# Kernel optimization log

Measured on AMD Instinct MI355X. Metric: run time of the kernel, lower is better.

The kernel has to match this reference:

```python
import jax, jax.numpy as jnp
import numpy as np

N = 50000       # n_nodes
E = 800000      # n_edges
DIN = 64
DH = 64
DOUT = 64


def setup_inputs() -> dict:
    key = jax.random.key(0)
    k0, k1, k2, k3, k4 = jax.random.split(key, 5)
    x = jax.random.normal(k0, (N, DIN), dtype=jnp.float32)
    edge_index = jax.random.randint(k1, (2, E), 0, N, dtype=jnp.int32)
    # learnable per-edge weight (nn.Parameter); positive init keeps gcn_norm well-defined
    edge_weight = jax.random.uniform(k2, (E,), jnp.float32, 0.1, 1.0)
    W1 = jax.random.normal(k3, (DH, DIN), dtype=jnp.float32) * (1.0 / np.sqrt(DIN))
    b1 = jnp.zeros((DH,), jnp.float32)
    W2 = jax.random.normal(k4, (DOUT, DH), dtype=jnp.float32) * (1.0 / np.sqrt(DH))
    b2 = jnp.zeros((DOUT,), jnp.float32)
    return {"x": x, "edge_weight": edge_weight, "W1": W1, "b1": b1,
            "W2": W2, "b2": b2, "edge_index": edge_index}


def _gcn_norm(edge_index, edge_weight, n):
    # PyG gcn_norm: add self-loops (weight 1), symmetric normalization.
    loop = jnp.arange(n, dtype=edge_index.dtype)
    row = jnp.concatenate([edge_index[0], loop])   # source nodes
    col = jnp.concatenate([edge_index[1], loop])   # target nodes
    w = jnp.concatenate([edge_weight, jnp.ones((n,), edge_weight.dtype)])
    deg = jax.ops.segment_sum(w, col, num_segments=n)
    dinv = jnp.where(deg > 0, jax.lax.rsqrt(jnp.where(deg > 0, deg, 1.0)), 0.0)
    norm = dinv[row] * w * dinv[col]               # [E + N]
    return row, col, norm


def _gcn_layer(x, W, b, row, col, norm, n):
    h = x @ W.T                                     # [N, out]
    # gather source features, scale by norm, scatter-add into targets
    out = jax.ops.segment_sum(h[row] * norm[:, None], col, num_segments=n)
    return out + b


def reference(x, edge_weight, W1, b1, W2, b2, edge_index):
    n = x.shape[0]
    row, col, norm = _gcn_norm(edge_index, edge_weight, n)
    h = _gcn_layer(x, W1, b1, row, col, norm, n)
    h = jax.nn.relu(h)                              # self.pre: ReLU + Dropout (identity in eval)
    return _gcn_layer(h, W2, b2, row, col, norm, n)
```

## Files before the change

### kernel.cpp

```cpp
#include <hip/hip_runtime.h>

#define D 64
#define GN 128
#define SW 68
#define SX 132
#define MAXDEG 64
#define RBITS_C 8
#define RANGE_C 256
#define MAXB_C 5120
#define RANGE_F 64
#define APB 2048

typedef unsigned long long u64;
typedef unsigned int u32;
typedef unsigned short u16;
typedef unsigned char u8;

__device__ __forceinline__ float4 fma4(float4 w, float s, float4 c) {
    c.x = fmaf(w.x, s, c.x); c.y = fmaf(w.y, s, c.y);
    c.z = fmaf(w.z, s, c.z); c.w = fmaf(w.w, s, c.w);
    return c;
}

__device__ __forceinline__ u32 f2bf(float f) {
    u32 u = __float_as_uint(f);
    return (u + 0x7FFFu + ((u >> 16) & 1u)) >> 16;
}
__device__ __forceinline__ u32 pack2(float a, float b) { return f2bf(a) | (f2bf(b) << 16); }
__device__ __forceinline__ float blo(u32 u) { return __uint_as_float(u << 16); }
__device__ __forceinline__ float bhi(u32 u) { return __uint_as_float(u & 0xFFFF0000u); }

__global__ __launch_bounds__(256) void k_g1b(
        const float* __restrict__ in, const float* __restrict__ W,
        u16* __restrict__ h, int N, int GG,
        const int* __restrict__ ei, const float* __restrict__ ew,
        u64* __restrict__ barr, u32* __restrict__ gcount, int E, int NB) {
    __shared__ __align__(16) char smem[51200];
    int t = threadIdx.x;

    if ((int)blockIdx.x < GG) {
        float* sWt = (float*)smem;
        float* sxT = (float*)(smem + 17408);
        int node0 = blockIdx.x * GN;

        for (int i = t; i < D * D / 4; i += 256) {
            int j = i >> 4, k4 = i & 15;
            float4 w = ((const float4*)W)[i];
            sWt[(4 * k4 + 0) * SW + j] = w.x;
            sWt[(4 * k4 + 1) * SW + j] = w.y;
            sWt[(4 * k4 + 2) * SW + j] = w.z;
            sWt[(4 * k4 + 3) * SW + j] = w.w;
        }
        for (int i = t; i < GN * D / 4; i += 256) {
            int nn = i >> 4, k4 = i & 15;
            int n = node0 + nn;
            float4 v = make_float4(0.f, 0.f, 0.f, 0.f);
            if (n < N) v = ((const float4*)(in + (size_t)n * D))[k4];
            sxT[(4 * k4 + 0) * SX + nn] = v.x;
            sxT[(4 * k4 + 1) * SX + nn] = v.y;
            sxT[(4 * k4 + 2) * SX + nn] = v.z;
            sxT[(4 * k4 + 3) * SX + nn] = v.w;
        }
        __syncthreads();

        int jg = (t & 7) * 8;
        int ng = (t >> 3) * 4;
        float4 a0[4], a1[4];
        #pragma unroll
        for (int a = 0; a < 4; ++a) {
            a0[a] = make_float4(0.f, 0.f, 0.f, 0.f);
            a1[a] = make_float4(0.f, 0.f, 0.f, 0.f);
        }

        #pragma unroll 8
        for (int k = 0; k < D; ++k) {
            const float* wr = &sWt[k * SW + jg];
            float4 w0 = *(const float4*)wr;
            float4 w1 = *(const float4*)(wr + 4);
            float4 xv = *(const float4*)&sxT[k * SX + ng];
            a0[0] = fma4(w0, xv.x, a0[0]);  a1[0] = fma4(w1, xv.x, a1[0]);
            a0[1] = fma4(w0, xv.y, a0[1]);  a1[1] = fma4(w1, xv.y, a1[1]);
            a0[2] = fma4(w0, xv.z, a0[2]);  a1[2] = fma4(w1, xv.z, a1[2]);
            a0[3] = fma4(w0, xv.w, a0[3]);  a1[3] = fma4(w1, xv.w, a1[3]);
        }

        #pragma unroll
        for (int a = 0; a < 4; ++a) {
            int n = node0 + ng + a;
            if (n >= N) continue;
            uint4 st;
            st.x = pack2(a0[a].x, a0[a].y);
            st.y = pack2(a0[a].z, a0[a].w);
            st.z = pack2(a1[a].x, a1[a].y);
            st.w = pack2(a1[a].z, a1[a].w);
            *(uint4*)(h + (size_t)n * D + jg) = st;
        }
    } else {
        u64* srec  = (u64*)smem;
        u8*  sbkt  = (u8*)(smem + 16384);
        u32* scnt  = (u32*)(smem + 18432);
        u32* sbase = (u32*)(smem + 19456);

        int e0 = (blockIdx.x - GG) * APB;
        int ne = min(APB, E - e0);

        for (int i = t; i < 256; i += 256) scnt[i] = 0;
        __syncthreads();

        for (int i = t; i < ne; i += 256) {
            int e   = e0 + i;
            int r   = ei[e];
            int c   = ei[(size_t)E + e];
            float w = ew[e];
            int b   = c >> RBITS_C;
            srec[i] = ((u64)__float_as_uint(w) << 32)
                    | (u32)r | ((u32)(c & (RANGE_C - 1)) << 20);
            sbkt[i] = (u8)b;
            atomicAdd(&scnt[b], 1u);
        }
        __syncthreads();

        for (int i = t; i < NB; i += 256) {
            u32 cnt = scnt[i];
            sbase[i] = cnt ? atomicAdd(&gcount[i], cnt) : 0u;
            scnt[i] = 0;
        }
        __syncthreads();

        for (int i = t; i < ne; i += 256) {
            int b   = sbkt[i];
            u32 rk  = atomicAdd(&scnt[b], 1u);
            u32 pos = sbase[b] + rk;
            if (pos < MAXB_C) barr[(size_t)b * MAXB_C + pos] = srec[i];
        }
    }
}

__global__ __launch_bounds__(256) void k_csr(
        const u64* __restrict__ barr, const u32* __restrict__ gcount,
        u64* __restrict__ degcnt, int2* __restrict__ eg, int N) {
    __shared__ __align__(16) int2 seg[RANGE_F * MAXDEG];
    __shared__ u32   scnt[RANGE_F];
    __shared__ float sdeg[RANGE_F];

    int fb = blockIdx.x;
    int cb = fb >> 2;
    int sub = fb & 3;
    int t = threadIdx.x;
    u32 cnt = min(gcount[cb], (u32)MAXB_C);
    int base_c = fb << 6;

    if (t < RANGE_F) { scnt[t] = 0; sdeg[t] = 1.0f; }
    __syncthreads();

    const u64* bp = barr + (size_t)cb * MAXB_C;
    for (u32 i = t; i < cnt; i += 256) {
        u64 rec = bp[i];
        int cl8 = (int)((rec >> 20) & 0xFFu);
        if ((cl8 >> 6) != sub) continue;
        int cl  = cl8 & (RANGE_F - 1);
        int src = (int)(rec & 0xFFFFFu);
        u32 wb  = (u32)(rec >> 32);
        u32 rank = atomicAdd(&scnt[cl], 1u);
        atomicAdd(&sdeg[cl], __uint_as_float(wb));
        if (rank < MAXDEG) seg[(cl << 6) + rank] = make_int2(src, (int)wb);
    }
    __syncthreads();

    if (t < RANGE_F) {
        int n = base_c + t;
        if (n < N) {
            u32 c2 = min(scnt[t], (u32)MAXDEG);
            float dd = rsqrtf(sdeg[t]);
            degcnt[n] = ((u64)c2 << 32) | (u64)__float_as_uint(dd);
        }
    }

    int nt = min(RANGE_F, N - base_c);
    const int4* s4 = (const int4*)seg;
    int4* d4 = (int4*)(eg + ((size_t)base_c << 6));
    int tot = nt << 5;
    for (int i = t; i < tot; i += 256) {
        int cl = i >> 5;
        int lv = (int)min(scnt[cl], (u32)MAXDEG);
        if (((i & 31) << 1) < lv) d4[i] = s4[i];
    }
}

__global__ __launch_bounds__(256) void k_gemmb(
        const float* __restrict__ in, const float* __restrict__ W,
        const float* __restrict__ bias, float* __restrict__ out, int N) {
    __shared__ __align__(16) float sWt[D * SW];
    __shared__ __align__(16) float sxT[D * SX];

    int t = threadIdx.x;
    int node0 = blockIdx.x * GN;

    for (int i = t; i < D * D / 4; i += 256) {
        int j = i >> 4, k4 = i & 15;
        float4 w = ((const float4*)W)[i];
        sWt[(4 * k4 + 0) * SW + j] = w.x;
        sWt[(4 * k4 + 1) * SW + j] = w.y;
        sWt[(4 * k4 + 2) * SW + j] = w.z;
        sWt[(4 * k4 + 3) * SW + j] = w.w;
    }
    for (int i = t; i < GN * D / 4; i += 256) {
        int nn = i >> 4, k4 = i & 15;
        int n = node0 + nn;
        float4 v = make_float4(0.f, 0.f, 0.f, 0.f);
        if (n < N) v = ((const float4*)(in + (size_t)n * D))[k4];
        sxT[(4 * k4 + 0) * SX + nn] = v.x;
        sxT[(4 * k4 + 1) * SX + nn] = v.y;
        sxT[(4 * k4 + 2) * SX + nn] = v.z;
        sxT[(4 * k4 + 3) * SX + nn] = v.w;
    }
    __syncthreads();

    int jg = (t & 7) * 8;
    int ng = (t >> 3) * 4;
    float4 bb0 = *(const float4*)(bias + jg);
    float4 bb1 = *(const float4*)(bias + jg + 4);
    float4 a0[4], a1[4];
    #pragma unroll
    for (int a = 0; a < 4; ++a) { a0[a] = bb0; a1[a] = bb1; }

    #pragma unroll 8
    for (int k = 0; k < D; ++k) {
        const float* wr = &sWt[k * SW + jg];
        float4 w0 = *(const float4*)wr;
        float4 w1 = *(const float4*)(wr + 4);
        float4 xv = *(const float4*)&sxT[k * SX + ng];
        a0[0] = fma4(w0, xv.x, a0[0]);  a1[0] = fma4(w1, xv.x, a1[0]);
        a0[1] = fma4(w0, xv.y, a0[1]);  a1[1] = fma4(w1, xv.y, a1[1]);
        a0[2] = fma4(w0, xv.z, a0[2]);  a1[2] = fma4(w1, xv.z, a1[2]);
        a0[3] = fma4(w0, xv.w, a0[3]);  a1[3] = fma4(w1, xv.w, a1[3]);
    }

    #pragma unroll
    for (int a = 0; a < 4; ++a) {
        int n = node0 + ng + a;
        if (n >= N) continue;
        float* o = out + (size_t)n * D + jg;
        *(float4*)o       = a0[a];
        *(float4*)(o + 4) = a1[a];
    }
}

template<bool FOLD>
__device__ __forceinline__ void gather8(
        const u16* __restrict__ h, const u64* __restrict__ degcnt,
        int2* __restrict__ eg, float4 bia, float4 bib,
        u64* __restrict__ se, int n, int lane, float acc[8]) {
    int g = lane >> 3;
    int f = (lane & 7) * 8;
    const u32* dv = (const u32*)degcnt;
    size_t s = (size_t)n << 6;

    int2 ee = eg[s + lane];
    u64 dcn = degcnt[n];
    int c = min((int)(dcn >> 32), MAXDEG);
    float dinv_n = __uint_as_float((u32)dcn);

    if (lane < c) {
        float wf;
        if (FOLD) {
            wf = __int_as_float(ee.y);
        } else {
            float di = __uint_as_float(dv[(size_t)ee.x << 1]);
            wf = __int_as_float(ee.y) * di * dinv_n;
            eg[s + lane] = make_int2(ee.x, __float_as_int(wf));
        }
        se[lane] = ((u64)__float_as_uint(wf) << 32) | (u32)ee.x;
    }

    #pragma unroll
    for (int i = 0; i < 8; ++i) acc[i] = 0.f;

    if (g == 0) {
        float d2 = dinv_n * dinv_n;
        uint4 hv = *(const uint4*)(h + s + f);
        acc[0] = fmaf(blo(hv.x), d2, bia.x); acc[1] = fmaf(bhi(hv.x), d2, bia.y);
        acc[2] = fmaf(blo(hv.y), d2, bia.z); acc[3] = fmaf(bhi(hv.y), d2, bia.w);
        acc[4] = fmaf(blo(hv.z), d2, bib.x); acc[5] = fmaf(bhi(hv.z), d2, bib.y);
        acc[6] = fmaf(blo(hv.w), d2, bib.z); acc[7] = fmaf(bhi(hv.w), d2, bib.w);
    }

    u64 recs[8];
    #pragma unroll
    for (int k = 0; k < 8; ++k) {
        int e = g + (k << 3);
        if (e < c) recs[k] = se[e];
    }
    uint4 hv[8];
    #pragma unroll
    for (int k = 0; k < 8; ++k) {
        int e = g + (k << 3);
        if (e < c)
            hv[k] = *(const uint4*)(h + ((size_t)(u32)recs[k] << 6) + f);
    }
    #pragma unroll
    for (int k = 0; k < 8; ++k) {
        int e = g + (k << 3);
        if (e < c) {
            float w = __uint_as_float((u32)(recs[k] >> 32));
            acc[0] = fmaf(blo(hv[k].x), w, acc[0]); acc[1] = fmaf(bhi(hv[k].x), w, acc[1]);
            acc[2] = fmaf(blo(hv[k].y), w, acc[2]); acc[3] = fmaf(bhi(hv[k].y), w, acc[3]);
            acc[4] = fmaf(blo(hv[k].z), w, acc[4]); acc[5] = fmaf(bhi(hv[k].z), w, acc[5]);
            acc[6] = fmaf(blo(hv[k].w), w, acc[6]); acc[7] = fmaf(bhi(hv[k].w), w, acc[7]);
        }
    }
}

__global__ __launch_bounds__(256) void k_agg_relu(
        const u16* __restrict__ h, const u64* __restrict__ degcnt,
        int2* __restrict__ eg, const float* __restrict__ b1,
        u16* __restrict__ h2, int N) {
    __shared__ u64 sedge[4][64];

    int t = threadIdx.x, wid = t >> 6, lane = t & 63;
    int n = blockIdx.x * 4 + wid;
    if (n >= N) return;
    int g = lane >> 3, f = (lane & 7) * 8;

    float4 bia = *(const float4*)(b1 + f);
    float4 bib = *(const float4*)(b1 + f + 4);

    float acc[8];
    gather8<false>(h, degcnt, eg, bia, bib, sedge[wid], n, lane, acc);

    #pragma unroll
    for (int k = 0; k < 8; ++k) {
        acc[k] += __shfl_xor(acc[k], 8);
        acc[k] += __shfl_xor(acc[k], 16);
        acc[k] += __shfl_xor(acc[k], 32);
    }

    if (g == 0) {
        uint4 st;
        st.x = pack2(fmaxf(acc[0], 0.f), fmaxf(acc[1], 0.f));
        st.y = pack2(fmaxf(acc[2], 0.f), fmaxf(acc[3], 0.f));
        st.z = pack2(fmaxf(acc[4], 0.f), fmaxf(acc[5], 0.f));
        st.w = pack2(fmaxf(acc[6], 0.f), fmaxf(acc[7], 0.f));
        *(uint4*)(h2 + ((size_t)n << 6) + f) = st;
    }
}

__global__ __launch_bounds__(256) void k_aggregate(
        const u16* __restrict__ h, const u64* __restrict__ degcnt,
        int2* __restrict__ eg, float* __restrict__ z, int N) {
    __shared__ u64 sedge[4][64];

    int t = threadIdx.x, wid = t >> 6, lane = t & 63;
    int n = blockIdx.x * 4 + wid;
    if (n >= N) return;
    int g = lane >> 3, f = (lane & 7) * 8;

    float4 zz = make_float4(0.f, 0.f, 0.f, 0.f);
    float acc[8];
    gather8<true>(h, degcnt, eg, zz, zz, sedge[wid], n, lane, acc);

    #pragma unroll
    for (int k = 0; k < 8; ++k) {
        acc[k] += __shfl_xor(acc[k], 8);
        acc[k] += __shfl_xor(acc[k], 16);
        acc[k] += __shfl_xor(acc[k], 32);
    }

    if (g == 0) {
        float* o = z + ((size_t)n << 6) + f;
        *(float4*)o       = make_float4(acc[0], acc[1], acc[2], acc[3]);
        *(float4*)(o + 4) = make_float4(acc[4], acc[5], acc[6], acc[7]);
    }
}

extern "C" void kernel_launch(void* const* d_in, const int* in_sizes, int n_in,
                              void* d_out, int out_size, void* d_ws, size_t ws_size,
                              hipStream_t stream) {
    const float* x  = (const float*)d_in[0];
    const float* ew = (const float*)d_in[1];
    const float* W1 = (const float*)d_in[2];
    const float* b1 = (const float*)d_in[3];
    const float* W2 = (const float*)d_in[4];
    const float* b2 = (const float*)d_in[5];
    const int*   ei = (const int*)d_in[6];

    int N = in_sizes[0] / D;
    int E = in_sizes[1];
    int NBC = (N + RANGE_C - 1) >> RBITS_C;
    int NBF = (N + RANGE_F - 1) / RANGE_F;
    float* out = (float*)d_out;

    char* p = (char*)d_ws;
    u64*   degcnt = (u64*)p;   p += (size_t)N * 8;
    int2*  eg     = (int2*)p;  p += (size_t)N * MAXDEG * 8;
    u16*   h      = (u16*)p;   p += (size_t)N * D * 2;
    u16*   h2     = (u16*)p;   p += (size_t)N * D * 2;
    float* z      = (float*)p; p += (size_t)N * D * 4;
    u64*   barr   = (u64*)p;   p += (size_t)NBC * MAXB_C * 8;
    u32*   gcount = (u32*)p;   p += 4096;

    dim3 blk(256);
    int gemm_grid   = (N + GN - 1) / GN;
    int bucket_grid = (E + APB - 1) / APB;
    int agg_grid    = (N + 3) / 4;

    hipMemsetAsync(gcount, 0, 4096, stream);

    k_g1b<<<dim3(gemm_grid + bucket_grid), blk, 0, stream>>>(
        x, W1, h, N, gemm_grid, ei, ew, barr, gcount, E, NBC);

    k_csr<<<dim3(NBF), blk, 0, stream>>>(barr, gcount, degcnt, eg, N);

    k_agg_relu<<<dim3(agg_grid), blk, 0, stream>>>(h, degcnt, eg, b1, h2, N);

    k_aggregate<<<dim3(agg_grid), blk, 0, stream>>>(h2, degcnt, eg, z, N);
    k_gemmb<<<dim3(gemm_grid), blk, 0, stream>>>(z, W2, b2, out, N);
}
```

Baseline: 171.9 us.

## Reorder layer-2 to GEMM-then-aggregate with bf16 intermediate and fused bias

Layer 2 now applies the weight matrix before aggregation, as the reference does. The GEMM reads bf16 h2 and writes a bf16 h3, and the final aggregation adds the bias and writes the fp32 output directly. This removes the fp32 z round trip through memory and halves the GEMM input and output traffic. It also splits the edge-list load so lanes 32-63 only read when the node has more than 32 edges, though this adds a dependency on the degree load and rounds the layer-2 pre-aggregation features to bf16.

```diff
diff --git a/kernel.cpp b/kernel.cpp
--- a/kernel.cpp
+++ b/kernel.cpp
@@ -187,9 +187,9 @@
     }
 }
 
-__global__ __launch_bounds__(256) void k_gemmb(
-        const float* __restrict__ in, const float* __restrict__ W,
-        const float* __restrict__ bias, float* __restrict__ out, int N) {
+__global__ __launch_bounds__(256) void k_gemm2(
+        const u16* __restrict__ in, const float* __restrict__ W,
+        u16* __restrict__ h3, int N) {
     __shared__ __align__(16) float sWt[D * SW];
     __shared__ __align__(16) float sxT[D * SX];
 
@@ -204,25 +204,27 @@
         sWt[(4 * k4 + 2) * SW + j] = w.z;
         sWt[(4 * k4 + 3) * SW + j] = w.w;
     }
-    for (int i = t; i < GN * D / 4; i += 256) {
-        int nn = i >> 4, k4 = i & 15;
+    for (int i = t; i < GN * D / 8; i += 256) {
+        int nn = i >> 3, k8 = i & 7;
         int n = node0 + nn;
-        float4 v = make_float4(0.f, 0.f, 0.f, 0.f);
-        if (n < N) v = ((const float4*)(in + (size_t)n * D))[k4];
-        sxT[(4 * k4 + 0) * SX + nn] = v.x;
-        sxT[(4 * k4 + 1) * SX + nn] = v.y;
-        sxT[(4 * k4 + 2) * SX + nn] = v.z;
-        sxT[(4 * k4 + 3) * SX + nn] = v.w;
+        uint4 v = make_uint4(0, 0, 0, 0);
+        if (n < N) v = ((const uint4*)(in + (size_t)n * D))[k8];
+        float* sx = &sxT[(8 * k8) * SX + nn];
+        sx[0 * SX] = blo(v.x); sx[1 * SX] = bhi(v.x);
+        sx[2 * SX] = blo(v.y); sx[3 * SX] = bhi(v.y);
+        sx[4 * SX] = blo(v.z); sx[5 * SX] = bhi(v.z);
+        sx[6 * SX] = blo(v.w); sx[7 * SX] = bhi(v.w);
     }
     __syncthreads();
 
     int jg = (t & 7) * 8;
     int ng = (t >> 3) * 4;
-    float4 bb0 = *(const float4*)(bias + jg);
-    float4 bb1 = *(const float4*)(bias + jg + 4);
     float4 a0[4], a1[4];
     #pragma unroll
-    for (int a = 0; a < 4; ++a) { a0[a] = bb0; a1[a] = bb1; }
+    for (int a = 0; a < 4; ++a) {
+        a0[a] = make_float4(0.f, 0.f, 0.f, 0.f);
+        a1[a] = make_float4(0.f, 0.f, 0.f, 0.f);
+    }
 
     #pragma unroll 8
     for (int k = 0; k < D; ++k) {
@@ -240,9 +242,12 @@
     for (int a = 0; a < 4; ++a) {
         int n = node0 + ng + a;
         if (n >= N) continue;
-        float* o = out + (size_t)n * D + jg;
-        *(float4*)o       = a0[a];
-        *(float4*)(o + 4) = a1[a];
+        uint4 st;
+        st.x = pack2(a0[a].x, a0[a].y);
+        st.y = pack2(a0[a].z, a0[a].w);
+        st.z = pack2(a1[a].x, a1[a].y);
+        st.w = pack2(a1[a].z, a1[a].w);
+        *(uint4*)(h3 + (size_t)n * D + jg) = st;
     }
 }
 
@@ -256,10 +261,12 @@
     const u32* dv = (const u32*)degcnt;
     size_t s = (size_t)n << 6;
 
-    int2 ee = eg[s + lane];
+    int2 ee = make_int2(0, 0);
+    if (lane < 32) ee = eg[s + lane];
     u64 dcn = degcnt[n];
     int c = min((int)(dcn >> 32), MAXDEG);
     float dinv_n = __uint_as_float((u32)dcn);
+    if (lane >= 32 && lane < c) ee = eg[s + lane];
 
     if (lane < c) {
         float wf;
@@ -345,9 +352,10 @@
     }
 }
 
-__global__ __launch_bounds__(256) void k_aggregate(
+__global__ __launch_bounds__(256) void k_agg_out(
         const u16* __restrict__ h, const u64* __restrict__ degcnt,
-        int2* __restrict__ eg, float* __restrict__ z, int N) {
+        int2* __restrict__ eg, const float* __restrict__ b,
+        float* __restrict__ out, int N) {
     __shared__ u64 sedge[4][64];
 
     int t = threadIdx.x, wid = t >> 6, lane = t & 63;
@@ -355,9 +363,11 @@
     if (n >= N) return;
     int g = lane >> 3, f = (lane & 7) * 8;
 
-    float4 zz = make_float4(0.f, 0.f, 0.f, 0.f);
+    float4 bia = *(const float4*)(b + f);
+    float4 bib = *(const float4*)(b + f + 4);
+
     float acc[8];
-    gather8<true>(h, degcnt, eg, zz, zz, sedge[wid], n, lane, acc);
+    gather8<true>(h, degcnt, eg, bia, bib, sedge[wid], n, lane, acc);
 
     #pragma unroll
     for (int k = 0; k < 8; ++k) {
@@ -367,7 +377,7 @@
     }
 
     if (g == 0) {
-        float* o = z + ((size_t)n << 6) + f;
+        float* o = out + ((size_t)n << 6) + f;
         *(float4*)o       = make_float4(acc[0], acc[1], acc[2], acc[3]);
         *(float4*)(o + 4) = make_float4(acc[4], acc[5], acc[6], acc[7]);
     }
@@ -395,7 +405,7 @@
     int2*  eg     = (int2*)p;  p += (size_t)N * MAXDEG * 8;
     u16*   h      = (u16*)p;   p += (size_t)N * D * 2;
     u16*   h2     = (u16*)p;   p += (size_t)N * D * 2;
-    float* z      = (float*)p; p += (size_t)N * D * 4;
+    u16*   h3     = (u16*)p;   p += (size_t)N * D * 2;
     u64*   barr   = (u64*)p;   p += (size_t)NBC * MAXB_C * 8;
     u32*   gcount = (u32*)p;   p += 4096;
 
@@ -413,6 +423,6 @@
 
     k_agg_relu<<<dim3(agg_grid), blk, 0, stream>>>(h, degcnt, eg, b1, h2, N);
 
-    k_aggregate<<<dim3(agg_grid), blk, 0, stream>>>(h2, degcnt, eg, z, N);
-    k_gemmb<<<dim3(gemm_grid), blk, 0, stream>>>(z, W2, b2, out, N);
-}
+    k_gemm2<<<dim3(gemm_grid), blk, 0, stream>>>(h2, W2, h3, N);
+    k_agg_out<<<dim3(agg_grid), blk, 0, stream>>>(h3, degcnt, eg, b2, out, N);
+}
```

Measured after the change: 168.4 us. 2.0% less time.
